# Performance work log

Measured on AMD Instinct MI355X. Metric: run time of the kernel, lower is better.

The kernel has to match this reference:

```python
import jax, jax.numpy as jnp
import numpy as np
from jax import lax

B, H, W, C = 8, 64, 64, 256
OUT = 1024          # channels (final conv filters)
KS = 3              # kernel_size
GROUP_DIV = 1
N_GROUPS = C // GROUP_DIV  # 256 -> depthwise-style grouped convs
DN = ('NHWC', 'HWIO', 'NHWC')
EPS = 1e-5


def setup_inputs() -> dict:
    key = jax.random.key(0)
    ks = jax.random.split(key, 6)
    x = jax.random.normal(ks[0], (B, H, W, C), jnp.float32)
    w_spatial = jax.random.normal(ks[1], (B, KS, KS, C // N_GROUPS, C), jnp.float32) * 0.05
    w_pointwise = jax.random.normal(ks[2], (B, 1, 1, C // N_GROUPS, C), jnp.float32) * 0.05
    bias = jax.random.normal(ks[3], (B, C), jnp.float32) * 0.05
    conv_w = jax.random.normal(ks[4], (KS, KS, C, OUT), jnp.float32) * (1.0 / np.sqrt(KS * KS * C))
    conv_b = jnp.zeros((OUT,), jnp.float32)
    return {"x": x, "w_spatial": w_spatial, "w_pointwise": w_pointwise,
            "bias": bias, "conv_w": conv_w, "conv_b": conv_b}


def _instance_norm(x):
    # TF: (x - mean) / (std + eps), population std over H,W per sample/channel
    mean = jnp.mean(x, axis=(1, 2), keepdims=True)
    std = jnp.sqrt(jnp.mean((x - mean) ** 2, axis=(1, 2), keepdims=True))
    return (x - mean) / (std + EPS)


def _per_sample(xi, ws, wp, b):
    # xi: [H,W,C]; ws: [ks,ks,1,C]; wp: [1,1,1,C]; b: [C]
    y = lax.conv_general_dilated(xi[None], ws, (1, 1), 'SAME',
                                 dimension_numbers=DN,
                                 feature_group_count=N_GROUPS)
    y = lax.conv_general_dilated(y, wp, (1, 1), 'VALID',
                                 dimension_numbers=DN,
                                 feature_group_count=N_GROUPS) + b
    return y[0]


def reference(x, w_spatial, w_pointwise, bias, conv_w, conv_b):
    x = _instance_norm(x)
    # batched per-sample dynamic grouped spatial + pointwise conv
    x = jax.vmap(_per_sample)(x, w_spatial, w_pointwise, bias)  # [B,H,W,C]
    # shared 3x3 SAME conv C -> OUT with bias
    y = lax.conv_general_dilated(x, conv_w, (1, 1), 'SAME',
                                 dimension_numbers=DN) + conv_b
    return y
```

## Files before the change

### kernel.cpp

```cpp
#include <hip/hip_runtime.h>
#include <hip/hip_bf16.h>
#include <cstdint>
#include <cstddef>

constexpr int Bn   = 8;
constexpr int Hn   = 64;
constexpr int Wn   = 64;
constexpr int Cn   = 256;
constexpr int OUTC = 1024;
constexpr int HPAD = 66;
constexpr int WPAD = 66;
#define EPS 1e-5f

typedef __attribute__((ext_vector_type(4))) float f32x4;
typedef __bf16 bf16x8 __attribute__((ext_vector_type(8)));

__device__ __forceinline__ void gload_lds16(const void* g, void* l) {
    __builtin_amdgcn_global_load_lds(
        (__attribute__((address_space(1))) void*)g,
        (__attribute__((address_space(3))) void*)l,
        16, 0, 0);
}

__global__ __launch_bounds__(256) void k0_transpose_w(const float* __restrict__ conv_w,
                                                      __hip_bfloat16* __restrict__ wT) {
    __shared__ float tile[64][65];
    const int tap = blockIdx.x;
    const int ct  = blockIdx.y;
    const int ot  = blockIdx.z;
    const int t   = threadIdx.x;
    const int lo  = t & 63;
    const int cq  = t >> 6;

#pragma unroll
    for (int k = 0; k < 16; ++k) {
        int ci = k * 4 + cq;
        tile[lo][ci] = conv_w[((size_t)(tap * Cn + ct * 64 + ci)) * OUTC + ot * 64 + lo];
    }
    __syncthreads();
#pragma unroll
    for (int k = 0; k < 16; ++k) {
        int oo = k * 4 + cq;
        wT[((size_t)(tap * OUTC + ot * 64 + oo)) * Cn + ct * 64 + lo] =
            __float2bfloat16(tile[oo][lo]);
    }
}

__global__ __launch_bounds__(1024) void k1_stats_partial(const float* __restrict__ x,
                                                         float* __restrict__ ps,
                                                         float* __restrict__ pq) {
    __shared__ float sb[2][4][256];
    const int bh = blockIdx.x;
    const int tid = threadIdx.x;
    const int c = tid & 255;
    const int s = tid >> 8;
    const float* row = x + (size_t)bh * Wn * Cn + (size_t)s * 16 * Cn + c;
    float sm = 0.f, q = 0.f;
#pragma unroll
    for (int w = 0; w < 16; ++w) {
        float v = row[(size_t)w * Cn];
        sm += v; q += v * v;
    }
    sb[0][s][c] = sm; sb[1][s][c] = q;
    __syncthreads();
    if (s == 0) {
        float S = 0.f, Q = 0.f;
#pragma unroll
        for (int k = 0; k < 4; ++k) { S += sb[0][k][c]; Q += sb[1][k][c]; }
        ps[bh * Cn + c] = S;
        pq[bh * Cn + c] = Q;
    }
}

__global__ __launch_bounds__(1024) void k2_stats_final(const float* __restrict__ ps,
                                                       const float* __restrict__ pq,
                                                       float* __restrict__ scale,
                                                       float* __restrict__ shift) {
    __shared__ float sb[2][4][256];
    const int b = blockIdx.x;
    const int tid = threadIdx.x;
    const int c = tid & 255;
    const int qd = tid >> 8;
    float S = 0.f, Q = 0.f;
#pragma unroll 4
    for (int i = 0; i < 16; ++i) {
        int h = qd * 16 + i;
        S += ps[(b * Hn + h) * Cn + c];
        Q += pq[(b * Hn + h) * Cn + c];
    }
    sb[0][qd][c] = S; sb[1][qd][c] = Q;
    __syncthreads();
    if (qd == 0) {
        float s2 = 0.f, q2 = 0.f;
#pragma unroll
        for (int k = 0; k < 4; ++k) { s2 += sb[0][k][c]; q2 += sb[1][k][c]; }
        const float inv = 1.f / (float)(Hn * Wn);
        float mean = s2 * inv;
        float var  = fmaxf(q2 * inv - mean * mean, 0.f);
        float sc   = 1.f / (sqrtf(var) + EPS);
        scale[b * Cn + c] = sc;
        shift[b * Cn + c] = -mean * sc;
    }
}

__global__ __launch_bounds__(256) void k3_dwconv(const float* __restrict__ x,
                                                 const float* __restrict__ w_sp,
                                                 const float* __restrict__ w_pw,
                                                 const float* __restrict__ bias,
                                                 const float* __restrict__ scale,
                                                 const float* __restrict__ shift,
                                                 __hip_bfloat16* __restrict__ tpad) {
    const int bq = blockIdx.x;
    const int wq = bq & 3;
    const int bh = bq >> 2;
    const int b  = bh / HPAD;
    const int hp = bh - b * HPAD;
    const int c  = threadIdx.x;
    __hip_bfloat16* orow = tpad + ((size_t)(b * HPAD + hp)) * WPAD * Cn + c;
    const __hip_bfloat16 z = __float2bfloat16(0.f);

    if (hp == 0 || hp == HPAD - 1) {
        int wlo = wq * 17, whi = wlo + 17 < WPAD ? wlo + 17 : WPAD;
        for (int wp = wlo; wp < whi; ++wp) orow[(size_t)wp * Cn] = z;
        return;
    }
    const int h = hp - 1;
    const float sc = scale[b * Cn + c];
    const float sh = shift[b * Cn + c];
    float w9[9];
#pragma unroll
    for (int k = 0; k < 9; ++k) w9[k] = w_sp[(b * 9 + k) * Cn + c];
    const float pw = w_pw[b * Cn + c];
    const float bv = bias[b * Cn + c];
    const float* xb = x + (size_t)b * Hn * Wn * Cn + c;

    bool rv[3];
#pragma unroll
    for (int r = 0; r < 3; ++r) { int rr = h - 1 + r; rv[r] = (rr >= 0 && rr < Hn); }

    if (wq == 0) orow[0] = z;
    if (wq == 3) orow[(size_t)(WPAD - 1) * Cn] = z;

    const int w0 = wq * 16;
    float win[3][3];
#pragma unroll
    for (int r = 0; r < 3; ++r) {
        win[r][0] = (rv[r] && w0 > 0)
                    ? (xb[((size_t)(h - 1 + r) * Wn + (w0 - 1)) * Cn] * sc + sh) : 0.f;
        win[r][1] = rv[r] ? (xb[((size_t)(h - 1 + r) * Wn + w0) * Cn] * sc + sh) : 0.f;
    }
    for (int i = 0; i < 16; ++i) {
        const int w = w0 + i;
#pragma unroll
        for (int r = 0; r < 3; ++r)
            win[r][2] = (rv[r] && (w + 1) < Wn)
                        ? (xb[((size_t)(h - 1 + r) * Wn + (w + 1)) * Cn] * sc + sh) : 0.f;
        float y = 0.f;
#pragma unroll
        for (int r = 0; r < 3; ++r)
#pragma unroll
            for (int qq = 0; qq < 3; ++qq)
                y += win[r][qq] * w9[r * 3 + qq];
        orow[(size_t)(w + 1) * Cn] = __float2bfloat16(y * pw + bv);
#pragma unroll
        for (int r = 0; r < 3; ++r) { win[r][0] = win[r][1]; win[r][1] = win[r][2]; }
    }
}

constexpr int KSTEPS = 72;
constexpr int BUFSZ  = 32768;

__global__ __launch_bounds__(512, 2) void k4_gemm(const __hip_bfloat16* __restrict__ tpad,
                                                  const __hip_bfloat16* __restrict__ wT,
                                                  const float* __restrict__ conv_b,
                                                  float* __restrict__ out) {
    __shared__ __align__(16) char smem[4 * BUFSZ];

    const int tid  = threadIdx.x;
    const int lane = tid & 63;
    const int wv   = tid >> 6;
    const int wm   = wv >> 2;
    const int wn   = wv & 3;
    const int g    = lane >> 4, l15 = lane & 15;

    const int bid = blockIdx.x;
    const int mt  = (bid & 7) * 16 + ((bid >> 3) & 15);
    const int nt  = bid >> 7;
    const int pixbase = mt * 256;
    const int b       = mt >> 4;
    const int hbase   = (mt & 15) * 4;
    const int obase   = nt * 256;

    int aoff[2], boff[2];
#pragma unroll
    for (int j = 0; j < 2; ++j) {
        int u = j * 512 + tid;
        int r = u >> 3, p = u & 7;
        int l = p ^ (r & 7);
        int pix = 2 * r + (l >> 2);
        int hh  = hbase + (pix >> 6);
        int ww  = pix & 63;
        aoff[j] = ((b * HPAD + hh) * WPAD + ww) * Cn + (l & 3) * 8;
        boff[j] = (obase + 2 * r + (l >> 2)) * Cn + (l & 3) * 8;
    }

    auto stageS = [&](int s) {
        const int tap = s >> 3, ks = s & 7;
        const int kh  = tap / 3, kw = tap - 3 * kh;
        const __hip_bfloat16* aS = tpad + ((kh * WPAD + kw) * Cn + ks * 32);
        const __hip_bfloat16* bS = wT + (size_t)tap * (OUTC * Cn) + ks * 32;
        char* buf = smem + (s & 3) * BUFSZ;
        gload_lds16(aS + aoff[0], buf + (size_t)(0 * 512 + wv * 64) * 16);
        gload_lds16(aS + aoff[1], buf + (size_t)(1 * 512 + wv * 64) * 16);
        gload_lds16(bS + boff[0], buf + 16384 + (size_t)(0 * 512 + wv * 64) * 16);
        gload_lds16(bS + boff[1], buf + 16384 + (size_t)(1 * 512 + wv * 64) * 16);
    };

    f32x4 acc[8][4] = {};

    stageS(0);
    stageS(1);

#pragma unroll 1
    for (int t = 0; t < KSTEPS; ++t) {
        if (t < KSTEPS - 1) { asm volatile("s_waitcnt vmcnt(4)" ::: "memory"); }
        else                { asm volatile("s_waitcnt vmcnt(0)" ::: "memory"); }
        __builtin_amdgcn_sched_barrier(0);
        __builtin_amdgcn_s_barrier();
        __builtin_amdgcn_sched_barrier(0);

        char* Ab = smem + (t & 3) * BUFSZ;
        char* Bb = Ab + 16384;

        bf16x8 bfr[4], af[8];
#pragma unroll
        for (int n = 0; n < 4; ++n) {
            int o = wn * 64 + n * 16 + l15;
            int r = o >> 1;
            bfr[n] = *(const bf16x8*)(Bb + r * 128 +
                         ((((o & 1) << 2) | g) ^ (r & 7)) * 16);
        }
#pragma unroll
        for (int m = 0; m < 8; ++m) {
            int pix = wm * 128 + m * 16 + l15;
            int r = pix >> 1;
            af[m] = *(const bf16x8*)(Ab + r * 128 +
                         ((((pix & 1) << 2) | g) ^ (r & 7)) * 16);
        }

        if (t + 2 < KSTEPS) stageS(t + 2);

        __builtin_amdgcn_s_setprio(1);
#pragma unroll
        for (int m = 0; m < 8; ++m)
#pragma unroll
            for (int n = 0; n < 4; ++n)
                acc[m][n] = __builtin_amdgcn_mfma_f32_16x16x32_bf16(
                    af[m], bfr[n], acc[m][n], 0, 0, 0);
        __builtin_amdgcn_s_setprio(0);
    }

    float cb[4];
#pragma unroll
    for (int n = 0; n < 4; ++n) cb[n] = conv_b[obase + wn * 64 + n * 16 + l15];
#pragma unroll
    for (int m = 0; m < 8; ++m) {
#pragma unroll
        for (int j = 0; j < 4; ++j) {
            int r = pixbase + wm * 128 + m * 16 + g * 4 + j;
            float* orow = out + (size_t)r * OUTC + obase + wn * 64 + l15;
#pragma unroll
            for (int n = 0; n < 4; ++n)
                orow[n * 16] = acc[m][n][j] + cb[n];
        }
    }
}

extern "C" void kernel_launch(void* const* d_in, const int* in_sizes, int n_in,
                              void* d_out, int out_size, void* d_ws, size_t ws_size,
                              hipStream_t stream) {
    const float* x      = (const float*)d_in[0];
    const float* w_sp   = (const float*)d_in[1];
    const float* w_pw   = (const float*)d_in[2];
    const float* bias   = (const float*)d_in[3];
    const float* conv_w = (const float*)d_in[4];
    const float* conv_b = (const float*)d_in[5];
    float* out = (float*)d_out;

    char* ws = (char*)d_ws;
    __hip_bfloat16* wT    = (__hip_bfloat16*)(ws);
    float*          ps    = (float*)(ws + 4718592);
    float*          pq    = (float*)(ws + 4718592 + 524288);
    float*          scale = (float*)(ws + 5767168);
    float*          shift = (float*)(ws + 5775360);
    __hip_bfloat16* tpad  = (__hip_bfloat16*)(ws + 5783552);

    k0_transpose_w<<<dim3(9, 4, 16), 256, 0, stream>>>(conv_w, wT);
    k1_stats_partial<<<Bn * Hn, 1024, 0, stream>>>(x, ps, pq);
    k2_stats_final<<<Bn, 1024, 0, stream>>>(ps, pq, scale, shift);
    k3_dwconv<<<Bn * HPAD * 4, 256, 0, stream>>>(x, w_sp, w_pw, bias, scale, shift, tpad);
    k4_gemm<<<512, 512, 0, stream>>>(tpad, wT, conv_b, out);
}
```

Measured before the change: 176.5 us.

## Switch GEMM to 32x32x16 MFMA and sync once per two k-steps

The convolution GEMM inner loop now issues 32x32x16 bf16 MFMAs on larger accumulator fragments instead of 16x16x32 ones, with a new epilogue row mapping to match. The k-loop is also unrolled into pairs of substeps that share one waitcnt and barrier, so there are half as many block-wide synchronisations. The aim is fewer MFMA issues and less barrier stall time. In exchange, each barrier now waits for all outstanding prefetches (vmcnt(0)), which shortens the effective prefetch overlap.

```diff
diff --git a/kernel.cpp b/kernel.cpp
--- a/kernel.cpp
+++ b/kernel.cpp
@@ -12,7 +12,7 @@
 constexpr int WPAD = 66;
 #define EPS 1e-5f
 
-typedef __attribute__((ext_vector_type(4))) float f32x4;
+typedef __attribute__((ext_vector_type(16))) float f32x16;
 typedef __bf16 bf16x8 __attribute__((ext_vector_type(8)));
 
 __device__ __forceinline__ void gload_lds16(const void* g, void* l) {
@@ -181,7 +181,8 @@
     const int wv   = tid >> 6;
     const int wm   = wv >> 2;
     const int wn   = wv & 3;
-    const int g    = lane >> 4, l15 = lane & 15;
+    const int l31  = lane & 31;
+    const int kh2  = lane >> 5;
 
     const int bid = blockIdx.x;
     const int mt  = (bid & 7) * 16 + ((bid >> 3) & 15);
@@ -216,62 +217,74 @@
         gload_lds16(bS + boff[1], buf + 16384 + (size_t)(1 * 512 + wv * 64) * 16);
     };
 
-    f32x4 acc[8][4] = {};
+    f32x16 acc[4][2] = {};
+
+    auto substep = [&](int t, bool dostage) {
+        char* Ab = smem + (t & 3) * BUFSZ;
+        char* Bb = Ab + 16384;
+        bf16x8 bfr[2][2], af[4][2];
+#pragma unroll
+        for (int nf = 0; nf < 2; ++nf)
+#pragma unroll
+            for (int kk = 0; kk < 2; ++kk) {
+                int o = wn * 64 + nf * 32 + l31;
+                int r = o >> 1;
+                int slot = (((o & 1) << 2) | (kk * 2 + kh2)) ^ (r & 7);
+                bfr[nf][kk] = *(const bf16x8*)(Bb + r * 128 + slot * 16);
+            }
+#pragma unroll
+        for (int mf = 0; mf < 4; ++mf)
+#pragma unroll
+            for (int kk = 0; kk < 2; ++kk) {
+                int pix = wm * 128 + mf * 32 + l31;
+                int r = pix >> 1;
+                int slot = (((pix & 1) << 2) | (kk * 2 + kh2)) ^ (r & 7);
+                af[mf][kk] = *(const bf16x8*)(Ab + r * 128 + slot * 16);
+            }
+        if (dostage) stageS(t + 2);
+        __builtin_amdgcn_s_setprio(1);
+#pragma unroll
+        for (int mf = 0; mf < 4; ++mf)
+#pragma unroll
+            for (int nf = 0; nf < 2; ++nf)
+#pragma unroll
+                for (int kk = 0; kk < 2; ++kk)
+                    acc[mf][nf] = __builtin_amdgcn_mfma_f32_32x32x16_bf16(
+                        af[mf][kk], bfr[nf][kk], acc[mf][nf], 0, 0, 0);
+        __builtin_amdgcn_s_setprio(0);
+    };
 
     stageS(0);
     stageS(1);
+    asm volatile("s_waitcnt vmcnt(0)" ::: "memory");
+    __builtin_amdgcn_s_barrier();
+    __builtin_amdgcn_sched_barrier(0);
 
 #pragma unroll 1
-    for (int t = 0; t < KSTEPS; ++t) {
-        if (t < KSTEPS - 1) { asm volatile("s_waitcnt vmcnt(4)" ::: "memory"); }
-        else                { asm volatile("s_waitcnt vmcnt(0)" ::: "memory"); }
+    for (int body = 0; body < KSTEPS / 2; ++body) {
+        const int t0 = 2 * body;
+        substep(t0,     t0 + 2 < KSTEPS);
+        substep(t0 + 1, t0 + 3 < KSTEPS);
         __builtin_amdgcn_sched_barrier(0);
-        __builtin_amdgcn_s_barrier();
-        __builtin_amdgcn_sched_barrier(0);
-
-        char* Ab = smem + (t & 3) * BUFSZ;
-        char* Bb = Ab + 16384;
-
-        bf16x8 bfr[4], af[8];
-#pragma unroll
-        for (int n = 0; n < 4; ++n) {
-            int o = wn * 64 + n * 16 + l15;
-            int r = o >> 1;
-            bfr[n] = *(const bf16x8*)(Bb + r * 128 +
-                         ((((o & 1) << 2) | g) ^ (r & 7)) * 16);
+        if (body + 1 < KSTEPS / 2) {
+            asm volatile("s_waitcnt vmcnt(0)" ::: "memory");
+            __builtin_amdgcn_s_barrier();
+            __builtin_amdgcn_sched_barrier(0);
         }
-#pragma unroll
-        for (int m = 0; m < 8; ++m) {
-            int pix = wm * 128 + m * 16 + l15;
-            int r = pix >> 1;
-            af[m] = *(const bf16x8*)(Ab + r * 128 +
-                         ((((pix & 1) << 2) | g) ^ (r & 7)) * 16);
-        }
-
-        if (t + 2 < KSTEPS) stageS(t + 2);
-
-        __builtin_amdgcn_s_setprio(1);
-#pragma unroll
-        for (int m = 0; m < 8; ++m)
-#pragma unroll
-            for (int n = 0; n < 4; ++n)
-                acc[m][n] = __builtin_amdgcn_mfma_f32_16x16x32_bf16(
-                    af[m], bfr[n], acc[m][n], 0, 0, 0);
-        __builtin_amdgcn_s_setprio(0);
-    }
-
-    float cb[4];
-#pragma unroll
-    for (int n = 0; n < 4; ++n) cb[n] = conv_b[obase + wn * 64 + n * 16 + l15];
-#pragma unroll
-    for (int m = 0; m < 8; ++m) {
-#pragma unroll
-        for (int j = 0; j < 4; ++j) {
-            int r = pixbase + wm * 128 + m * 16 + g * 4 + j;
-            float* orow = out + (size_t)r * OUTC + obase + wn * 64 + l15;
-#pragma unroll
-            for (int n = 0; n < 4; ++n)
-                orow[n * 16] = acc[m][n][j] + cb[n];
+    }
+
+    float cb[2];
+#pragma unroll
+    for (int nf = 0; nf < 2; ++nf) cb[nf] = conv_b[obase + wn * 64 + nf * 32 + l31];
+#pragma unroll
+    for (int mf = 0; mf < 4; ++mf) {
+#pragma unroll
+        for (int j = 0; j < 16; ++j) {
+            int row = (j & 3) + 8 * (j >> 2) + 4 * kh2;
+            int r = pixbase + wm * 128 + mf * 32 + row;
+            float* orow = out + (size_t)r * OUTC + obase + wn * 64 + l31;
+            orow[0]  = acc[mf][0][j] + cb[0];
+            orow[32] = acc[mf][1][j] + cb[1];
         }
     }
 }
```

Measured after the change: 188.4 us. 1.07x slower.

## Software-pipeline LDS fragment reads with MFMA and deepen global prefetch to three stages

Applied to the files above, without the earlier changes.

Restructures the conv GEMM main loop so the A fragments for the next k-step are read from LDS while the current step's MFMAs run, using double-buffered register arrays, and B fragments are loaded column by column between MFMA groups. Global-to-LDS staging is deepened from two steps ahead to three, with one barrier per step placed at its end. The goal is to hide LDS read latency and global load latency behind matrix-core work. In exchange it uses more VGPRs for the extra fragment buffers and hard-codes the step count of 72.

```diff
diff --git a/kernel.cpp b/kernel.cpp
--- a/kernel.cpp
+++ b/kernel.cpp
@@ -216,53 +216,88 @@
         gload_lds16(bS + boff[1], buf + 16384 + (size_t)(1 * 512 + wv * 64) * 16);
     };
 
+    const int slot = ((((l15 & 1) << 2) | g) ^ ((l15 >> 1) & 7)) * 16;
+    const int aRd  = wm * 8192 + (l15 >> 1) * 128 + slot;
+    const int bRd  = 16384 + wn * 4096 + (l15 >> 1) * 128 + slot;
+
     f32x4 acc[8][4] = {};
-
-    stageS(0);
-    stageS(1);
+    bf16x8 A0[8], A1[8];
+
+    stageS(0); stageS(1); stageS(2);
+    asm volatile("s_waitcnt vmcnt(4)" ::: "memory");
+    __builtin_amdgcn_s_barrier();
+    __builtin_amdgcn_sched_barrier(0);
+    {
+        char* b0p = smem;
+#pragma unroll
+        for (int m = 0; m < 8; ++m)
+            A0[m] = *(const bf16x8*)(b0p + aRd + m * 1024);
+    }
+
+#define COLG(n_, b_)                                                          \
+    {                                                                         \
+        _Pragma("unroll")                                                     \
+        for (int m = 0; m < 8; ++m)                                           \
+            acc[m][n_] = __builtin_amdgcn_mfma_f32_16x16x32_bf16(             \
+                aC[m], b_, acc[m][n_], 0, 0, 0);                              \
+    }
+
+    auto step = [&](int t, bf16x8 (&aC)[8], bf16x8 (&aN)[8],
+                    bool st, bool rd, bool tail) {
+        char* cb = smem + (t & 3) * BUFSZ;
+        char* nb = smem + ((t + 1) & 3) * BUFSZ;
+        if (st) stageS(t + 3);
+        bf16x8 b0 = *(const bf16x8*)(cb + bRd + 0 * 1024);
+        bf16x8 b1 = *(const bf16x8*)(cb + bRd + 1 * 1024);
+        if (rd) aN[0] = *(const bf16x8*)(nb + aRd + 0 * 1024);
+        __builtin_amdgcn_s_setprio(1);
+        __builtin_amdgcn_sched_barrier(0);
+        COLG(0, b0);
+        __builtin_amdgcn_sched_barrier(0);
+        bf16x8 b2 = *(const bf16x8*)(cb + bRd + 2 * 1024);
+        if (rd) {
+            aN[1] = *(const bf16x8*)(nb + aRd + 1 * 1024);
+            aN[2] = *(const bf16x8*)(nb + aRd + 2 * 1024);
+        }
+        COLG(1, b1);
+        __builtin_amdgcn_sched_barrier(0);
+        bf16x8 b3 = *(const bf16x8*)(cb + bRd + 3 * 1024);
+        if (rd) {
+            aN[3] = *(const bf16x8*)(nb + aRd + 3 * 1024);
+            aN[4] = *(const bf16x8*)(nb + aRd + 4 * 1024);
+        }
+        COLG(2, b2);
+        __builtin_amdgcn_sched_barrier(0);
+        if (rd) {
+            aN[5] = *(const bf16x8*)(nb + aRd + 5 * 1024);
+            aN[6] = *(const bf16x8*)(nb + aRd + 6 * 1024);
+            aN[7] = *(const bf16x8*)(nb + aRd + 7 * 1024);
+        }
+        COLG(3, b3);
+        __builtin_amdgcn_s_setprio(0);
+        if (tail) {
+            __builtin_amdgcn_sched_barrier(0);
+            if (st) { asm volatile("s_waitcnt vmcnt(4)" ::: "memory"); }
+            else    { asm volatile("s_waitcnt vmcnt(0)" ::: "memory"); }
+            __builtin_amdgcn_s_barrier();
+            __builtin_amdgcn_sched_barrier(0);
+        }
+    };
 
 #pragma unroll 1
-    for (int t = 0; t < KSTEPS; ++t) {
-        if (t < KSTEPS - 1) { asm volatile("s_waitcnt vmcnt(4)" ::: "memory"); }
-        else                { asm volatile("s_waitcnt vmcnt(0)" ::: "memory"); }
-        __builtin_amdgcn_sched_barrier(0);
-        __builtin_amdgcn_s_barrier();
-        __builtin_amdgcn_sched_barrier(0);
-
-        char* Ab = smem + (t & 3) * BUFSZ;
-        char* Bb = Ab + 16384;
-
-        bf16x8 bfr[4], af[8];
-#pragma unroll
-        for (int n = 0; n < 4; ++n) {
-            int o = wn * 64 + n * 16 + l15;
-            int r = o >> 1;
-            bfr[n] = *(const bf16x8*)(Bb + r * 128 +
-                         ((((o & 1) << 2) | g) ^ (r & 7)) * 16);
-        }
-#pragma unroll
-        for (int m = 0; m < 8; ++m) {
-            int pix = wm * 128 + m * 16 + l15;
-            int r = pix >> 1;
-            af[m] = *(const bf16x8*)(Ab + r * 128 +
-                         ((((pix & 1) << 2) | g) ^ (r & 7)) * 16);
-        }
-
-        if (t + 2 < KSTEPS) stageS(t + 2);
-
-        __builtin_amdgcn_s_setprio(1);
-#pragma unroll
-        for (int m = 0; m < 8; ++m)
-#pragma unroll
-            for (int n = 0; n < 4; ++n)
-                acc[m][n] = __builtin_amdgcn_mfma_f32_16x16x32_bf16(
-                    af[m], bfr[n], acc[m][n], 0, 0, 0);
-        __builtin_amdgcn_s_setprio(0);
-    }
-
-    float cb[4];
-#pragma unroll
-    for (int n = 0; n < 4; ++n) cb[n] = conv_b[obase + wn * 64 + n * 16 + l15];
+    for (int tt = 0; tt < 68; tt += 2) {
+        step(tt,     A0, A1, true, true, true);
+        step(tt + 1, A1, A0, true, true, true);
+    }
+    step(68, A0, A1, true,  true,  true);
+    step(69, A1, A0, false, true,  true);
+    step(70, A0, A1, false, true,  true);
+    step(71, A1, A0, false, false, false);
+#undef COLG
+
+    float cb2[4];
+#pragma unroll
+    for (int n = 0; n < 4; ++n) cb2[n] = conv_b[obase + wn * 64 + n * 16 + l15];
 #pragma unroll
     for (int m = 0; m < 8; ++m) {
 #pragma unroll
@@ -271,7 +306,7 @@
             float* orow = out + (size_t)r * OUTC + obase + wn * 64 + l15;
 #pragma unroll
             for (int n = 0; n < 4; ++n)
-                orow[n * 16] = acc[m][n][j] + cb[n];
+                orow[n * 16] = acc[m][n][j] + cb2[n];
         }
     }
 }
```

Measured after the change: 172.5 us. 2.3% less time.

## Split GEMM k-step into two phases interleaving global staging with MFMA

Applied to the files above, without the earlier changes.

Restructures the main implicit-GEMM loop so each k-step runs in two halves. The A-fragment LDS reads and the MFMAs are split into two groups of four, and the A and B global-to-LDS loads for step t+2 are issued separately, one per half. LDS read addresses are precomputed once outside the loop. The goal is to overlap global loads, LDS reads and MFMA execution more finely and to lower register pressure, at the cost of extra barriers per iteration.

```diff
diff --git a/kernel.cpp b/kernel.cpp
--- a/kernel.cpp
+++ b/kernel.cpp
@@ -204,65 +204,90 @@
         boff[j] = (obase + 2 * r + (l >> 2)) * Cn + (l & 3) * 8;
     }
 
-    auto stageS = [&](int s) {
+    auto stageHalf = [&](int s, int half) {
         const int tap = s >> 3, ks = s & 7;
         const int kh  = tap / 3, kw = tap - 3 * kh;
-        const __hip_bfloat16* aS = tpad + ((kh * WPAD + kw) * Cn + ks * 32);
-        const __hip_bfloat16* bS = wT + (size_t)tap * (OUTC * Cn) + ks * 32;
         char* buf = smem + (s & 3) * BUFSZ;
-        gload_lds16(aS + aoff[0], buf + (size_t)(0 * 512 + wv * 64) * 16);
-        gload_lds16(aS + aoff[1], buf + (size_t)(1 * 512 + wv * 64) * 16);
-        gload_lds16(bS + boff[0], buf + 16384 + (size_t)(0 * 512 + wv * 64) * 16);
-        gload_lds16(bS + boff[1], buf + 16384 + (size_t)(1 * 512 + wv * 64) * 16);
+        if (half == 0) {
+            const __hip_bfloat16* aS = tpad + ((kh * WPAD + kw) * Cn + ks * 32);
+            gload_lds16(aS + aoff[0], buf + (size_t)(0 * 512 + wv * 64) * 16);
+            gload_lds16(aS + aoff[1], buf + (size_t)(1 * 512 + wv * 64) * 16);
+        } else {
+            const __hip_bfloat16* bS = wT + (size_t)tap * (OUTC * Cn) + ks * 32;
+            gload_lds16(bS + boff[0], buf + 16384 + (size_t)(0 * 512 + wv * 64) * 16);
+            gload_lds16(bS + boff[1], buf + 16384 + (size_t)(1 * 512 + wv * 64) * 16);
+        }
     };
 
+    const int slot = ((((l15 & 1) << 2) | g) ^ ((l15 >> 1) & 7)) * 16;
+    const int aRd  = wm * 8192 + (l15 >> 1) * 128 + slot;
+    const int bRd  = 16384 + wn * 4096 + (l15 >> 1) * 128 + slot;
+
     f32x4 acc[8][4] = {};
 
-    stageS(0);
-    stageS(1);
+    stageHalf(0, 0); stageHalf(0, 1);
+    stageHalf(1, 0); stageHalf(1, 1);
+    asm volatile("s_waitcnt vmcnt(4)" ::: "memory");
+    __builtin_amdgcn_s_barrier();
+    __builtin_amdgcn_sched_barrier(0);
 
 #pragma unroll 1
     for (int t = 0; t < KSTEPS; ++t) {
-        if (t < KSTEPS - 1) { asm volatile("s_waitcnt vmcnt(4)" ::: "memory"); }
-        else                { asm volatile("s_waitcnt vmcnt(0)" ::: "memory"); }
+        char* cb = smem + (t & 3) * BUFSZ;
+        const bool st = (t + 2 < KSTEPS);
+        bf16x8 bfr[4], aP[4], aQ[4];
+
+        if (st) stageHalf(t + 2, 0);
+#pragma unroll
+        for (int n = 0; n < 4; ++n)
+            bfr[n] = *(const bf16x8*)(cb + bRd + n * 1024);
+#pragma unroll
+        for (int m = 0; m < 4; ++m)
+            aP[m] = *(const bf16x8*)(cb + aRd + m * 1024);
         __builtin_amdgcn_sched_barrier(0);
         __builtin_amdgcn_s_barrier();
-        __builtin_amdgcn_sched_barrier(0);
-
-        char* Ab = smem + (t & 3) * BUFSZ;
-        char* Bb = Ab + 16384;
-
-        bf16x8 bfr[4], af[8];
-#pragma unroll
-        for (int n = 0; n < 4; ++n) {
-            int o = wn * 64 + n * 16 + l15;
-            int r = o >> 1;
-            bfr[n] = *(const bf16x8*)(Bb + r * 128 +
-                         ((((o & 1) << 2) | g) ^ (r & 7)) * 16);
-        }
-#pragma unroll
-        for (int m = 0; m < 8; ++m) {
-            int pix = wm * 128 + m * 16 + l15;
-            int r = pix >> 1;
-            af[m] = *(const bf16x8*)(Ab + r * 128 +
-                         ((((pix & 1) << 2) | g) ^ (r & 7)) * 16);
-        }
-
-        if (t + 2 < KSTEPS) stageS(t + 2);
-
+        asm volatile("s_waitcnt lgkmcnt(0)" ::: "memory");
+        __builtin_amdgcn_sched_barrier(0);
         __builtin_amdgcn_s_setprio(1);
 #pragma unroll
-        for (int m = 0; m < 8; ++m)
+        for (int m = 0; m < 4; ++m)
 #pragma unroll
             for (int n = 0; n < 4; ++n)
                 acc[m][n] = __builtin_amdgcn_mfma_f32_16x16x32_bf16(
-                    af[m], bfr[n], acc[m][n], 0, 0, 0);
+                    aP[m], bfr[n], acc[m][n], 0, 0, 0);
         __builtin_amdgcn_s_setprio(0);
-    }
-
-    float cb[4];
-#pragma unroll
-    for (int n = 0; n < 4; ++n) cb[n] = conv_b[obase + wn * 64 + n * 16 + l15];
+        __builtin_amdgcn_sched_barrier(0);
+        __builtin_amdgcn_s_barrier();
+
+        if (st) stageHalf(t + 2, 1);
+#pragma unroll
+        for (int m = 0; m < 4; ++m)
+            aQ[m] = *(const bf16x8*)(cb + aRd + (m + 4) * 1024);
+        __builtin_amdgcn_sched_barrier(0);
+        __builtin_amdgcn_s_barrier();
+        asm volatile("s_waitcnt lgkmcnt(0)" ::: "memory");
+        __builtin_amdgcn_sched_barrier(0);
+        __builtin_amdgcn_s_setprio(1);
+#pragma unroll
+        for (int m = 0; m < 4; ++m)
+#pragma unroll
+            for (int n = 0; n < 4; ++n)
+                acc[m + 4][n] = __builtin_amdgcn_mfma_f32_16x16x32_bf16(
+                    aQ[m], bfr[n], acc[m + 4][n], 0, 0, 0);
+        __builtin_amdgcn_s_setprio(0);
+        __builtin_amdgcn_sched_barrier(0);
+
+        if (t + 1 < KSTEPS) {
+            if (st) { asm volatile("s_waitcnt vmcnt(4)" ::: "memory"); }
+            else    { asm volatile("s_waitcnt vmcnt(0)" ::: "memory"); }
+            __builtin_amdgcn_s_barrier();
+            __builtin_amdgcn_sched_barrier(0);
+        }
+    }
+
+    float cb2[4];
+#pragma unroll
+    for (int n = 0; n < 4; ++n) cb2[n] = conv_b[obase + wn * 64 + n * 16 + l15];
 #pragma unroll
     for (int m = 0; m < 8; ++m) {
 #pragma unroll
@@ -271,7 +296,7 @@
             float* orow = out + (size_t)r * OUTC + obase + wn * 64 + l15;
 #pragma unroll
             for (int n = 0; n < 4; ++n)
-                orow[n * 16] = acc[m][n][j] + cb[n];
+                orow[n * 16] = acc[m][n][j] + cb2[n];
         }
     }
 }
```

Measured after the change: 188.8 us. +7.0%, slower.
